# Kernel tuning notes

Measured on AMD Instinct MI355X. Metric: run time of the kernel, lower is better.

The kernel has to match this reference:

```python
import jax, jax.numpy as jnp
import numpy as np
from jax import lax

D_STATE = 16
D_CONV = 4
D_MODEL = 1024
D_INNER = 2048
DT_RANK = 64
SEQLEN = 2048
BATCH = 2


def setup_inputs() -> dict:
    key = jax.random.key(0)
    ks = jax.random.split(key, 8)
    hidden_states = jax.random.normal(ks[0], (SEQLEN, BATCH, D_MODEL), jnp.float32)
    W_in = jax.random.normal(ks[1], (2 * D_INNER, D_MODEL), jnp.float32) * (D_MODEL ** -0.5)
    conv_w = jax.random.normal(ks[2], (D_INNER, D_CONV), jnp.float32) * (D_CONV ** -0.5)
    conv_b = jnp.zeros((D_INNER,), jnp.float32)
    W_x = jax.random.normal(ks[3], (DT_RANK + 2 * D_STATE, D_INNER), jnp.float32) * (D_INNER ** -0.5)
    dt_init_std = DT_RANK ** -0.5
    W_dt = jax.random.uniform(ks[4], (D_INNER, DT_RANK), jnp.float32, -dt_init_std, dt_init_std)
    # dt bias init: inverse-softplus of dt ~ LogUniform(1e-3, 1e-1)
    dt = jnp.exp(jax.random.uniform(ks[5], (D_INNER,), jnp.float32) * (np.log(0.1) - np.log(0.001)) + np.log(0.001))
    dt = jnp.clip(dt, 1e-4, None)
    dt_bias = dt + jnp.log(-jnp.expm1(-dt))
    A_log = jnp.log(jnp.tile(jnp.arange(1, D_STATE + 1, dtype=jnp.float32)[None, :], (D_INNER, 1)))
    Dp = jnp.ones((D_INNER,), jnp.float32)
    W_out = jax.random.normal(ks[6], (D_MODEL, D_INNER), jnp.float32) * (D_INNER ** -0.5)
    return {"hidden_states": hidden_states, "W_in": W_in, "conv_w": conv_w, "conv_b": conv_b,
            "W_x": W_x, "W_dt": W_dt, "dt_bias": dt_bias, "A_log": A_log, "D": Dp, "W_out": W_out}


def _mamba_forward(hidden_states, W_in, conv_w, conv_b, W_x, W_dt, dt_bias, A_log, D, W_out):
    L, B, _ = hidden_states.shape
    d_inner, d_state = A_log.shape
    dt_rank = W_dt.shape[1]
    # in_proj: [L,B,D] -> [L,B,2*d_inner] -> [B,2*d_inner,L]
    xz = jnp.einsum('lbd,ed->lbe', hidden_states, W_in)
    xz = jnp.transpose(xz, (1, 2, 0))
    x, z = jnp.split(xz, 2, axis=1)  # each [B,d_inner,L]
    # causal depthwise conv1d + silu
    x = lax.conv_general_dilated(x, conv_w[:, None, :], (1,), [(D_CONV - 1, 0)],
                                 dimension_numbers=('NCH', 'OIH', 'NCH'),
                                 feature_group_count=d_inner)
    x = jax.nn.silu(x + conv_b[None, :, None])  # [B,d_inner,L]
    # x_proj over (b l) tokens
    x_bl = jnp.transpose(x, (0, 2, 1)).reshape(B * L, d_inner)  # (b l) d
    x_dbl = x_bl @ W_x.T  # [(b l), dt_rank + 2*d_state]
    dt_lr, Bm, Cm = jnp.split(x_dbl, [dt_rank, dt_rank + d_state], axis=-1)
    dt = (W_dt @ dt_lr.T).reshape(d_inner, B, L).transpose(1, 0, 2)  # [B,d_inner,L]
    Bm = Bm.reshape(B, L, d_state)  # [B,L,n]
    Cm = Cm.reshape(B, L, d_state)
    # selective scan (delta_softplus=True, delta_bias=dt_bias)
    A = -jnp.exp(A_log)  # [d_inner, n]
    delta = jax.nn.softplus(dt + dt_bias[None, :, None])  # [B,d,L]
    delta_t = jnp.transpose(delta, (2, 0, 1))  # [L,B,d]
    u_t = jnp.transpose(x, (2, 0, 1))          # [L,B,d]
    B_t = jnp.transpose(Bm, (1, 0, 2))         # [L,B,n]
    C_t = jnp.transpose(Cm, (1, 0, 2))         # [L,B,n]

    def step(state, inp):
        d_i, u_i, b_i, c_i = inp
        dA = jnp.exp(d_i[:, :, None] * A[None])           # [B,d,n]
        dBu = (d_i * u_i)[:, :, None] * b_i[:, None, :]   # [B,d,n]
        state = state * dA + dBu
        y = jnp.einsum('bdn,bn->bd', state, c_i)
        return state, y

    init = jnp.zeros((B, d_inner, d_state), delta.dtype)
    _, ys = lax.scan(step, init, (delta_t, u_t, B_t, C_t))  # ys [L,B,d]
    y = jnp.transpose(ys, (1, 0, 2))                         # [B,L,d]
    y = y + jnp.transpose(x, (0, 2, 1)) * D[None, None, :]
    y = y * jax.nn.silu(jnp.transpose(z, (0, 2, 1)))
    out = y @ W_out.T  # [B,L,d_model]
    return jnp.transpose(out, (1, 0, 2))  # [L,B,d_model]


def reference(hidden_states, W_in, conv_w, conv_b, W_x, W_dt, dt_bias, A_log, D, W_out):
    return _mamba_forward(hidden_states, W_in, conv_w, conv_b, W_x, W_dt, dt_bias, A_log, D, W_out)
```

## Files before the change

### kernel.cpp

```cpp
#include <hip/hip_runtime.h>
#include <hip/hip_bf16.h>


#define L_SEQ 2048
#define N_B   2
#define D_M   1024
#define D_I   2048
#define D_ST  16
#define R_DT  64
#define CHNK  16
#define CT    128
#define KS    8

using bf16 = __hip_bfloat16;
typedef unsigned short u16;
typedef unsigned int u32;
typedef u16 u16x8 __attribute__((ext_vector_type(8)));
typedef __bf16 bf16x8 __attribute__((ext_vector_type(8)));
typedef float f32x4 __attribute__((ext_vector_type(4)));

__device__ __forceinline__ float b2f(u16 u) {
    union { u32 i; float f; } x;
    x.i = ((u32)u) << 16;
    return x.f;
}
__device__ __forceinline__ u16 f2b(float f) {
    union { bf16 h; u16 s; } x;
    x.h = __float2bfloat16(f);
    return x.s;
}

__device__ __forceinline__ void load4(const float* p, float* o) {
    const float4 v = *(const float4*)p;
    o[0] = v.x; o[1] = v.y; o[2] = v.z; o[3] = v.w;
}
__device__ __forceinline__ void load4(const bf16* p, float* o) {
    const ushort4 v = *(const ushort4*)(const void*)p;
    o[0] = b2f(v.x); o[1] = b2f(v.y); o[2] = b2f(v.z); o[3] = b2f(v.w);
}

__device__ __forceinline__ float softplus_f(float x) {
    return (x > 20.f) ? x : log1pf(__expf(x));
}
__device__ __forceinline__ float silu_f(float x) {
    return x / (1.f + __expf(-x));
}

__device__ __forceinline__ void gl_lds16(const u16* g, u16* l) {
    __builtin_amdgcn_global_load_lds(
        (const __attribute__((address_space(1))) void*)g,
        (__attribute__((address_space(3))) void*)l, 16, 0, 0);
}

template <int EPI>
__global__ __launch_bounds__(256) void bgemm(
    const u16* __restrict__ A, int lda,
    const u16* __restrict__ Wb, int ldb, int K,
    u16* __restrict__ bd, float* __restrict__ fout,
    const float* __restrict__ bias)
{
    __shared__ u16 As[128 * 32];
    __shared__ u16 Bs[128 * 32];

    const int tid = threadIdx.x;
    const int m0 = blockIdx.x * 128;
    const int n0 = blockIdx.y * 128;
    const int w  = tid >> 6;
    const int ln = tid & 63;

    const int sr0 = (w << 4) + (ln >> 2);
    const int sr1 = sr0 + 64;
    const int sx  = ln & 3;
    const int qa0 = (sx - (sr0 >> 1)) & 3;
    const int qa1 = (sx - (sr1 >> 1)) & 3;

    const u16* ga0 = A  + (size_t)(m0 + sr0) * lda + qa0 * 8;
    const u16* ga1 = A  + (size_t)(m0 + sr1) * lda + qa1 * 8;
    const u16* gb0 = Wb + (size_t)(n0 + sr0) * ldb + qa0 * 8;
    const u16* gb1 = Wb + (size_t)(n0 + sr1) * ldb + qa1 * 8;
    u16* la0 = As + ((w << 4) + 0) * 32;
    u16* la1 = As + ((w << 4) + 64) * 32;
    u16* lb0 = Bs + ((w << 4) + 0) * 32;
    u16* lb1 = Bs + ((w << 4) + 64) * 32;

    const int wr = (w >> 1) << 6;
    const int wc = (w & 1) << 6;
    const int lm = ln & 15;
    const int qf = ln >> 4;
    int aoff[4], boff[4];
#pragma unroll
    for (int i = 0; i < 4; ++i) {
        const int ra = wr + i * 16 + lm;
        aoff[i] = ra * 32 + (((qf + (ra >> 1)) & 3) << 3);
        const int rb = wc + i * 16 + lm;
        boff[i] = rb * 32 + (((qf + (rb >> 1)) & 3) << 3);
    }

    f32x4 acc[4][4] = {};

    for (int k0 = 0; k0 < K; k0 += 32) {
        if (k0) __syncthreads();
        gl_lds16(ga0 + k0, la0);
        gl_lds16(ga1 + k0, la1);
        gl_lds16(gb0 + k0, lb0);
        gl_lds16(gb1 + k0, lb1);
        __syncthreads();

        bf16x8 af[4], bf[4];
#pragma unroll
        for (int i = 0; i < 4; ++i) af[i] = *(const bf16x8*)&As[aoff[i]];
#pragma unroll
        for (int j = 0; j < 4; ++j) bf[j] = *(const bf16x8*)&Bs[boff[j]];
#pragma unroll
        for (int i = 0; i < 4; ++i)
#pragma unroll
            for (int j = 0; j < 4; ++j)
                acc[i][j] = __builtin_amdgcn_mfma_f32_16x16x32_bf16(
                    af[i], bf[j], acc[i][j], 0, 0, 0);
    }

    const int qr = (ln >> 4) << 2;
    float bv[4];
    if (EPI == 2) {
#pragma unroll
        for (int j = 0; j < 4; ++j) bv[j] = bias[n0 + wc + j * 16 + lm];
    }
#pragma unroll
    for (int i = 0; i < 4; ++i) {
#pragma unroll
        for (int reg = 0; reg < 4; ++reg) {
            const int rg = m0 + wr + i * 16 + qr + reg;
            if (EPI == 0) {
                const int bb = rg & (N_B - 1);
                const int l = rg >> 1;
                const size_t t = (size_t)bb * L_SEQ + l;
#pragma unroll
                for (int j = 0; j < 4; ++j)
                    bd[t * D_I + n0 + wc + j * 16 + lm] = f2b(acc[i][j][reg]);
            } else if (EPI == 1) {
                const int bb = rg >> 11;
                const int l = rg & (L_SEQ - 1);
                const size_t o = ((size_t)l * N_B + bb) * D_M;
#pragma unroll
                for (int j = 0; j < 4; ++j)
                    fout[o + n0 + wc + j * 16 + lm] = acc[i][j][reg];
            } else {
                const size_t t = (size_t)rg;
#pragma unroll
                for (int j = 0; j < 4; ++j)
                    bd[t * D_I + n0 + wc + j * 16 + lm] =
                        f2b(softplus_f(acc[i][j][reg] + bv[j]));
            }
        }
    }
}

__global__ __launch_bounds__(256) void xproj_k(
    const u16* __restrict__ u, const u16* __restrict__ Wxb,
    float* __restrict__ Part)
{
    __shared__ u16 As[64 * 32];
    __shared__ u16 Bs[96 * 264];

    const int tid = threadIdx.x;
    const int m0 = blockIdx.x * 64;
    const int kc = blockIdx.y;
    const int kbase = kc * 256;

    for (int e = tid; e < 96 * 32; e += 256) {
        const int row = e >> 5, kq = e & 31;
        const u16x8 v = *(const u16x8*)(Wxb + (size_t)row * D_I + kbase + kq * 8);
        *(u16x8*)&Bs[row * 264 + kq * 8] = v;
    }

    const int w  = tid >> 6;
    const int ln = tid & 63;
    const int sr = (w << 4) + (ln >> 2);
    const int sx = ln & 3;
    const int qa = (sx - (sr >> 1)) & 3;
    const u16* ga = u + (size_t)(m0 + sr) * D_I + kbase + qa * 8;
    u16* la = As + (w << 9);

    const int lm = ln & 15;
    const int qf = ln >> 4;
    const int ra = (w << 4) + lm;
    const int aoff = ra * 32 + (((qf + (ra >> 1)) & 3) << 3);

    f32x4 acc[6] = {};

    for (int it = 0; it < 8; ++it) {
        if (it) __syncthreads();
        gl_lds16(ga + it * 32, la);
        __syncthreads();

        const bf16x8 af = *(const bf16x8*)&As[aoff];
#pragma unroll
        for (int j = 0; j < 6; ++j) {
            const bf16x8 bf = *(const bf16x8*)&Bs[(j * 16 + lm) * 264 + it * 32 + qf * 8];
            acc[j] = __builtin_amdgcn_mfma_f32_16x16x32_bf16(af, bf, acc[j], 0, 0, 0);
        }
    }

    const int qr = (ln >> 4) << 2;
#pragma unroll
    for (int j = 0; j < 6; ++j) {
#pragma unroll
        for (int reg = 0; reg < 4; ++reg) {
            const int t = m0 + (w << 4) + qr + reg;
            Part[((size_t)kc * (N_B * L_SEQ) + t) * 96 + j * 16 + lm] = acc[j][reg];
        }
    }
}

__global__ __launch_bounds__(256) void xreduce(
    const float* __restrict__ Part, u16* __restrict__ dtlr,
    float* __restrict__ Bm, float* __restrict__ Cm)
{
    const int e = blockIdx.x * 256 + threadIdx.x;
    const int t = e / 96, c = e - t * 96;
    float s = 0.f;
#pragma unroll
    for (int kc = 0; kc < KS; ++kc)
        s += Part[(size_t)kc * (N_B * L_SEQ * 96) + e];
    if (c < 64)      dtlr[t * 64 + c] = f2b(s);
    else if (c < 80) Bm[t * 16 + (c - 64)] = s;
    else             Cm[t * 16 + (c - 80)] = s;
}

__global__ __launch_bounds__(256) void cvt_k(const float* __restrict__ s,
                                             u16* __restrict__ d)
{
    const size_t i = ((size_t)blockIdx.x * 256 + threadIdx.x) * 8;
    const float4 a = *(const float4*)(s + i);
    const float4 b = *(const float4*)(s + i + 4);
    u16 t[8] = {f2b(a.x), f2b(a.y), f2b(a.z), f2b(a.w),
                f2b(b.x), f2b(b.y), f2b(b.z), f2b(b.w)};
    *(u16x8*)(d + i) = *(const u16x8*)t;
}

__global__ __launch_bounds__(256) void gate_k(u16* __restrict__ y,
                                              const u16* __restrict__ z)
{
    const size_t i = ((size_t)blockIdx.x * 256 + threadIdx.x) * 8;
    u16x8 yv = *(u16x8*)(y + i);
    const u16x8 zv = *(const u16x8*)(z + i);
    u16 t[8];
#pragma unroll
    for (int j = 0; j < 8; ++j)
        t[j] = f2b(b2f(yv[j]) * silu_f(b2f(zv[j])));
    *(u16x8*)(y + i) = *(const u16x8*)t;
}

__global__ __launch_bounds__(256) void conv_k(
    const bf16* __restrict__ x, const float* __restrict__ cw,
    const float* __restrict__ cb, bf16* __restrict__ xc)
{
    const int t = blockIdx.x;
    const int l = t & (L_SEQ - 1);
#pragma unroll
    for (int it = 0; it < 2; ++it) {
        const int d = ((int)threadIdx.x + it * 256) << 2;
        float w[4][4], bias[4], acc[4];
#pragma unroll
        for (int dd = 0; dd < 4; ++dd)
            load4(cw + (size_t)(d + dd) * 4, w[dd]);
        load4(cb + d, bias);
#pragma unroll
        for (int dd = 0; dd < 4; ++dd) acc[dd] = bias[dd];
#pragma unroll
        for (int j = 0; j < 4; ++j) {
            const int ll = l - 3 + j;
            if (ll >= 0) {
                float xv[4];
                load4(x + (size_t)(t - 3 + j) * D_I + d, xv);
#pragma unroll
                for (int dd = 0; dd < 4; ++dd)
                    acc[dd] = fmaf(xv[dd], w[dd][j], acc[dd]);
            }
        }
        const ushort4 v = make_ushort4(f2b(silu_f(acc[0])), f2b(silu_f(acc[1])),
                                       f2b(silu_f(acc[2])), f2b(silu_f(acc[3])));
        *(ushort4*)(void*)(xc + (size_t)t * D_I + d) = v;
    }
}

template <int PHASE>
__global__ __launch_bounds__(256) void scan_chunk(
    bf16* __restrict__ dy, const bf16* __restrict__ u,
    const float* __restrict__ Bm, const float* __restrict__ Cm,
    const float* __restrict__ Alog, const float* __restrict__ Dp,
    float* __restrict__ Pc, float* __restrict__ Qc,
    const float* __restrict__ Sin)
{
    __shared__ u32 duS[CT * 64];
    __shared__ float Bs[CT][D_ST];
    __shared__ float Cs[(PHASE == 1) ? CT : 1][D_ST];

    const int tid = threadIdx.x;
    const int d0 = blockIdx.x * 64;
    const int b  = blockIdx.y;
    const int c  = blockIdx.z;
    const int row0 = b * L_SEQ + c * CT;

    for (int e = tid; e < CT * 8; e += 256) {
        const int l = e >> 3, g = e & 7;
        const size_t go = (size_t)(row0 + l) * D_I + d0 + g * 8;
        const u16x8 d8 = *(const u16x8*)((const u16*)dy + go);
        const u16x8 u8 = *(const u16x8*)((const u16*)u + go);
        u32 w[8];
#pragma unroll
        for (int j = 0; j < 8; ++j)
            w[j] = (u32)d8[j] | ((u32)u8[j] << 16);
        *(uint4*)&duS[l * 64 + g * 8]     = make_uint4(w[0], w[1], w[2], w[3]);
        *(uint4*)&duS[l * 64 + g * 8 + 4] = make_uint4(w[4], w[5], w[6], w[7]);
    }
    {
        const float4* src = (const float4*)(Bm + (size_t)row0 * D_ST);
        float4* dst = (float4*)Bs;
        for (int e = tid; e < CT * D_ST / 4; e += 256) dst[e] = src[e];
        if (PHASE == 1) {
            const float4* s2 = (const float4*)(Cm + (size_t)row0 * D_ST);
            float4* d2 = (float4*)Cs;
            for (int e = tid; e < CT * D_ST / 4; e += 256) d2[e] = s2[e];
        }
    }
    __syncthreads();

    const int dl = tid >> 2;
    const int d  = d0 + dl;
    const int ns = tid & 3;
    const size_t pqbase = (((size_t)b * CHNK + c) * D_I + d) * D_ST + ns * 4;

    float Av[4];
    {
        const float4 a4 = *(const float4*)(Alog + (size_t)d * D_ST + ns * 4);
        Av[0] = -__expf(a4.x); Av[1] = -__expf(a4.y);
        Av[2] = -__expf(a4.z); Av[3] = -__expf(a4.w);
    }

    float st[4] = {0.f, 0.f, 0.f, 0.f};
    float P[4]  = {1.f, 1.f, 1.f, 1.f};
    if (PHASE == 1) {
        const float4 s0 = *(const float4*)(Sin + pqbase);
        st[0] = s0.x; st[1] = s0.y; st[2] = s0.z; st[3] = s0.w;
    }
    const float Dd = (PHASE == 1) ? Dp[d] : 0.f;

    u32 w0 = duS[dl];
    u32 w1 = duS[64 + dl];

#pragma unroll 2
    for (int l = 0; l < CT; ++l) {
        const int lp = (l + 2 < CT) ? (l + 2) : (CT - 1);
        const u32 wn = duS[lp * 64 + dl];

        union { u32 i; float f; } dvv, uvv;
        dvv.i = w0 << 16;
        uvv.i = w0 & 0xFFFF0000u;
        const float dv = dvv.f, uv = uvv.f;
        const float dvu = dv * uv;

        float bn[4], cn[4] = {0.f, 0.f, 0.f, 0.f};
        {
            const float4 b4 = *(const float4*)&Bs[l][ns * 4];
            bn[0] = b4.x; bn[1] = b4.y; bn[2] = b4.z; bn[3] = b4.w;
        }
        if (PHASE == 1) {
            const float4 c4 = *(const float4*)&Cs[l][ns * 4];
            cn[0] = c4.x; cn[1] = c4.y; cn[2] = c4.z; cn[3] = c4.w;
        }

        float y = 0.f;
#pragma unroll
        for (int j = 0; j < 4; ++j) {
            const float dA = __expf(dv * Av[j]);
            if (PHASE == 0) P[j] *= dA;
            st[j] = fmaf(st[j], dA, dvu * bn[j]);
            if (PHASE == 1) y = fmaf(st[j], cn[j], y);
        }
        if (PHASE == 1) {
            y += __shfl_xor(y, 1);
            y += __shfl_xor(y, 2);
            if (ns == 0)
                ((u16*)duS)[(l * 64 + dl) * 2] = f2b(y + uv * Dd);
        }
        w0 = w1; w1 = wn;
    }

    if (PHASE == 0) {
        *(float4*)(Pc + pqbase) = make_float4(P[0], P[1], P[2], P[3]);
        *(float4*)(Qc + pqbase) = make_float4(st[0], st[1], st[2], st[3]);
    } else {
        __syncthreads();
        for (int e = tid; e < CT * 8; e += 256) {
            const int l = e >> 3, g = e & 7;
            u16 t[8];
#pragma unroll
            for (int j = 0; j < 8; ++j)
                t[j] = (u16)(duS[l * 64 + g * 8 + j] & 0xFFFFu);
            *(u16x8*)((u16*)dy + (size_t)(row0 + l) * D_I + d0 + g * 8) =
                *(const u16x8*)t;
        }
    }
}

__global__ __launch_bounds__(256) void scan_comb(
    const float* __restrict__ Pc, const float* __restrict__ Qc,
    float* __restrict__ Sin)
{
    const int b = blockIdx.y;
    const int d = blockIdx.x * 16 + (threadIdx.x >> 4);
    const int n = threadIdx.x & 15;
    float s = 0.f;
#pragma unroll
    for (int c = 0; c < CHNK; ++c) {
        const size_t idx = (((size_t)b * CHNK + c) * D_I + d) * D_ST + n;
        Sin[idx] = s;
        s = fmaf(s, Pc[idx], Qc[idx]);
    }
}

__global__ void zfill(float* o) {
    o[(size_t)blockIdx.x * 256 + threadIdx.x] = 0.f;
}

extern "C" void kernel_launch(void* const* d_in, const int* in_sizes, int n_in,
                              void* d_out, int out_size, void* d_ws, size_t ws_size,
                              hipStream_t stream)
{
    const float* hs   = (const float*)d_in[0];
    const float* Win  = (const float*)d_in[1];
    const float* cw   = (const float*)d_in[2];
    const float* cb   = (const float*)d_in[3];
    const float* Wx   = (const float*)d_in[4];
    const float* Wdt  = (const float*)d_in[5];
    const float* dtb  = (const float*)d_in[6];
    const float* Alog = (const float*)d_in[7];
    const float* Dp   = (const float*)d_in[8];
    const float* Wout = (const float*)d_in[9];
    float* out = (float*)d_out;

    const size_t SZ = (size_t)N_B * L_SEQ * D_I;
    const size_t NT = (size_t)N_B * L_SEQ;
    const size_t NHS   = NT * D_M;
    const size_t NWIN  = (size_t)2 * D_I * D_M;
    const size_t NWOUT = (size_t)D_M * D_I;
    const size_t NWX   = (size_t)96 * D_I;
    const size_t NWDT  = (size_t)D_I * R_DT;
    const size_t NEED = SZ * 2 * sizeof(bf16)
                      + (NHS + NWIN + NWOUT + NWX + NWDT + NT * R_DT) * sizeof(u16)
                      + NT * 2 * D_ST * sizeof(float);
    if (ws_size < NEED) {
        zfill<<<dim3((unsigned)((size_t)out_size / 256)), 256, 0, stream>>>(out);
        return;
    }

    bf16* RA   = (bf16*)d_ws;
    bf16* RB   = RA + SZ;
    u16* bhs   = (u16*)(RB + SZ);
    u16* bWin  = bhs + NHS;
    u16* bWout = bWin + NWIN;
    u16* bWx   = bWout + NWOUT;
    u16* bWdt  = bWx + NWX;
    u16* dtlr  = bWdt + NWDT;
    float* Bm  = (float*)(dtlr + NT * R_DT);
    float* Cm  = Bm + NT * D_ST;
    float* Part = out;
    const size_t PQ = (size_t)N_B * CHNK * D_I * D_ST;
    float* Pc  = out;
    float* Qc  = Pc + PQ;
    float* Sin = Qc + PQ;

    cvt_k<<<dim3((unsigned)(NHS / 2048)), 256, 0, stream>>>(hs, bhs);
    cvt_k<<<dim3((unsigned)(NWIN / 2048)), 256, 0, stream>>>(Win, bWin);
    cvt_k<<<dim3((unsigned)(NWOUT / 2048)), 256, 0, stream>>>(Wout, bWout);
    cvt_k<<<dim3((unsigned)(NWX / 2048)), 256, 0, stream>>>(Wx, bWx);
    cvt_k<<<dim3((unsigned)(NWDT / 2048)), 256, 0, stream>>>(Wdt, bWdt);
    bgemm<0><<<dim3(32, 16), 256, 0, stream>>>(
        bhs, D_M, bWin, D_M, D_M, (u16*)RA, nullptr, nullptr);
    conv_k<<<dim3(N_B * L_SEQ), 256, 0, stream>>>(RA, cw, cb, RB);
    xproj_k<<<dim3(64, KS), 256, 0, stream>>>((const u16*)RB, bWx, Part);
    xreduce<<<dim3((unsigned)(NT * 96 / 256)), 256, 0, stream>>>(Part, dtlr, Bm, Cm);
    bgemm<2><<<dim3(32, 16), 256, 0, stream>>>(
        dtlr, R_DT, bWdt, R_DT, R_DT, (u16*)RA, nullptr, dtb);
    scan_chunk<0><<<dim3(D_I / 64, N_B, CHNK), 256, 0, stream>>>(
        RA, RB, Bm, Cm, Alog, Dp, Pc, Qc, nullptr);
    scan_comb<<<dim3(D_I / 16, N_B), 256, 0, stream>>>(Pc, Qc, Sin);
    scan_chunk<1><<<dim3(D_I / 64, N_B, CHNK), 256, 0, stream>>>(
        RA, RB, Bm, Cm, Alog, Dp, nullptr, nullptr, Sin);
    bgemm<0><<<dim3(32, 16), 256, 0, stream>>>(
        bhs, D_M, bWin + (size_t)D_I * D_M, D_M, D_M, (u16*)RB, nullptr, nullptr);
    gate_k<<<dim3((unsigned)(SZ / 2048)), 256, 0, stream>>>((u16*)RA, (const u16*)RB);
    bgemm<1><<<dim3(32, 8), 256, 0, stream>>>(
        (const u16*)RA, D_I, bWout, D_I, D_I, nullptr, out, nullptr);
}
```

Baseline: 375.3 us.

## Halve scan chunk length, pad shared rows, batch combine loads, alias Sin onto Pc

Doubles the number of scan chunks (CT 128→64, CHNK 16→32), which doubles the grid of the chunked scan kernels and halves the serial recurrence length per block. Shared-memory rows are padded to 68 words to cut bank conflicts, and the software prefetch of the next du values is dropped in favour of direct LDS reads. The combine kernel now loads all P/Q values up front so the loads can be in flight together, and writes Sin in place over Pc (restrict removed) to fit the larger P/Q buffers in the output scratch. The cost is more P/Q traffic and a longer combine pass.

```diff
diff --git a/kernel.cpp b/kernel.cpp
--- a/kernel.cpp
+++ b/kernel.cpp
@@ -8,9 +8,10 @@
 #define D_I   2048
 #define D_ST  16
 #define R_DT  64
-#define CHNK  16
-#define CT    128
+#define CHNK  32
+#define CT    64
 #define KS    8
+#define DUS   68
 
 using bf16 = __hip_bfloat16;
 typedef unsigned short u16;
@@ -292,7 +293,7 @@
     float* __restrict__ Pc, float* __restrict__ Qc,
     const float* __restrict__ Sin)
 {
-    __shared__ u32 duS[CT * 64];
+    __shared__ u32 duS[CT * DUS];
     __shared__ float Bs[CT][D_ST];
     __shared__ float Cs[(PHASE == 1) ? CT : 1][D_ST];
 
@@ -311,8 +312,8 @@
 #pragma unroll
         for (int j = 0; j < 8; ++j)
             w[j] = (u32)d8[j] | ((u32)u8[j] << 16);
-        *(uint4*)&duS[l * 64 + g * 8]     = make_uint4(w[0], w[1], w[2], w[3]);
-        *(uint4*)&duS[l * 64 + g * 8 + 4] = make_uint4(w[4], w[5], w[6], w[7]);
+        *(uint4*)&duS[l * DUS + g * 8]     = make_uint4(w[0], w[1], w[2], w[3]);
+        *(uint4*)&duS[l * DUS + g * 8 + 4] = make_uint4(w[4], w[5], w[6], w[7]);
     }
     {
         const float4* src = (const float4*)(Bm + (size_t)row0 * D_ST);
@@ -346,14 +347,9 @@
     }
     const float Dd = (PHASE == 1) ? Dp[d] : 0.f;
 
-    u32 w0 = duS[dl];
-    u32 w1 = duS[64 + dl];
-
 #pragma unroll 2
     for (int l = 0; l < CT; ++l) {
-        const int lp = (l + 2 < CT) ? (l + 2) : (CT - 1);
-        const u32 wn = duS[lp * 64 + dl];
-
+        const u32 w0 = duS[l * DUS + dl];
         union { u32 i; float f; } dvv, uvv;
         dvv.i = w0 << 16;
         uvv.i = w0 & 0xFFFF0000u;
@@ -382,9 +378,8 @@
             y += __shfl_xor(y, 1);
             y += __shfl_xor(y, 2);
             if (ns == 0)
-                ((u16*)duS)[(l * 64 + dl) * 2] = f2b(y + uv * Dd);
-        }
-        w0 = w1; w1 = wn;
+                ((u16*)duS)[(l * DUS + dl) * 2] = f2b(y + uv * Dd);
+        }
     }
 
     if (PHASE == 0) {
@@ -397,7 +392,7 @@
             u16 t[8];
 #pragma unroll
             for (int j = 0; j < 8; ++j)
-                t[j] = (u16)(duS[l * 64 + g * 8 + j] & 0xFFFFu);
+                t[j] = (u16)(duS[l * DUS + g * 8 + j] & 0xFFFFu);
             *(u16x8*)((u16*)dy + (size_t)(row0 + l) * D_I + d0 + g * 8) =
                 *(const u16x8*)t;
         }
@@ -405,18 +400,25 @@
 }
 
 __global__ __launch_bounds__(256) void scan_comb(
-    const float* __restrict__ Pc, const float* __restrict__ Qc,
-    float* __restrict__ Sin)
+    const float* Pc, const float* Qc, float* Sin)
 {
     const int b = blockIdx.y;
     const int d = blockIdx.x * 16 + (threadIdx.x >> 4);
     const int n = threadIdx.x & 15;
+    const size_t i0 = (((size_t)b * CHNK) * D_I + d) * D_ST + n;
+    const size_t cs = (size_t)D_I * D_ST;
+
+    float p[CHNK], q[CHNK];
+#pragma unroll
+    for (int c = 0; c < CHNK; ++c) {
+        p[c] = Pc[i0 + c * cs];
+        q[c] = Qc[i0 + c * cs];
+    }
     float s = 0.f;
 #pragma unroll
     for (int c = 0; c < CHNK; ++c) {
-        const size_t idx = (((size_t)b * CHNK + c) * D_I + d) * D_ST + n;
-        Sin[idx] = s;
-        s = fmaf(s, Pc[idx], Qc[idx]);
+        Sin[i0 + c * cs] = s;
+        s = fmaf(s, p[c], q[c]);
     }
 }
 
@@ -469,7 +471,7 @@
     const size_t PQ = (size_t)N_B * CHNK * D_I * D_ST;
     float* Pc  = out;
     float* Qc  = Pc + PQ;
-    float* Sin = Qc + PQ;
+    float* Sin = Pc;
 
     cvt_k<<<dim3((unsigned)(NHS / 2048)), 256, 0, stream>>>(hs, bhs);
     cvt_k<<<dim3((unsigned)(NWIN / 2048)), 256, 0, stream>>>(Win, bWin);
```

Result: faster. 357.6 us (-4.7%).
